# Optimization experiments

Measured on AMD Instinct MI355X. Metric: run time of the kernel, lower is better.

Reference implementation:

```python
import jax, jax.numpy as jnp
import numpy as np

N, E, G = 100000, 1600000, 128
IN, HID, HEADS, EDIM, OUT = 16, 32, 4, 8, 4
HC = HEADS * HID


def _p(k, shape):
    return jax.random.normal(k, shape, jnp.float32) * 0.1


def setup_inputs():
    key = jax.random.key(0)
    ks = list(jax.random.split(key, 24))
    nxt = iter(ks)
    d = dict(
        x=jax.random.normal(next(nxt), (N, IN), jnp.float32),
        edge_index=jax.random.randint(next(nxt), (2, E), 0, N),
        edge_attr=jax.random.normal(next(nxt), (E, EDIM), jnp.float32),
        batch=jnp.sort(jax.random.randint(next(nxt), (N,), 0, G)),
    )
    # conv1: in=IN -> heads*hid
    d['wl1'] = _p(next(nxt), (IN, HC));  d['bl1'] = jnp.zeros((HC,), jnp.float32)
    d['wr1'] = _p(next(nxt), (IN, HC));  d['br1'] = jnp.zeros((HC,), jnp.float32)
    d['we1'] = _p(next(nxt), (EDIM, HC)); d['att1'] = _p(next(nxt), (HEADS, HID)); d['bc1'] = jnp.zeros((HC,), jnp.float32)
    # conv2: in=HC -> heads*hid
    d['wl2'] = _p(next(nxt), (HC, HC));  d['bl2'] = jnp.zeros((HC,), jnp.float32)
    d['wr2'] = _p(next(nxt), (HC, HC));  d['br2'] = jnp.zeros((HC,), jnp.float32)
    d['we2'] = _p(next(nxt), (EDIM, HC)); d['att2'] = _p(next(nxt), (HEADS, HID)); d['bc2'] = jnp.zeros((HC,), jnp.float32)
    # conv3: in=HC -> 1*hid (heads=1)
    d['wl3'] = _p(next(nxt), (HC, HID)); d['bl3'] = jnp.zeros((HID,), jnp.float32)
    d['wr3'] = _p(next(nxt), (HC, HID)); d['br3'] = jnp.zeros((HID,), jnp.float32)
    d['we3'] = _p(next(nxt), (EDIM, HID)); d['att3'] = _p(next(nxt), (1, HID)); d['bc3'] = jnp.zeros((HID,), jnp.float32)
    d['w_fc1'] = _p(next(nxt), (HID, 2 * HID)); d['b_fc1'] = jnp.zeros((2 * HID,), jnp.float32)
    d['w_fc2'] = _p(next(nxt), (2 * HID, OUT)); d['b_fc2'] = jnp.zeros((OUT,), jnp.float32)
    return d


def _gatv2(x, src, dst, eattr, wl, bl, wr, br, we, att, bias, n):
    # PyG GATv2Conv: e_ij = a^T . leaky_relu(Wl x_j + Wr x_i + We e_ij)
    H, C = att.shape
    xl = (x @ wl + bl).reshape(-1, H, C)  # source transform [N,H,C]
    xr = (x @ wr + br).reshape(-1, H, C)  # target transform [N,H,C]
    ea = (eattr @ we).reshape(-1, H, C)   # edge transform   [E,H,C]
    e = jax.nn.leaky_relu(xl[src] + xr[dst] + ea, 0.2)  # [E,H,C]
    logit = jnp.einsum('ehc,hc->eh', e, att)            # [E,H]
    m = jax.ops.segment_max(logit, dst, num_segments=n)
    p = jnp.exp(logit - m[dst])
    s = jax.ops.segment_sum(p, dst, num_segments=n)
    alpha = p / (s[dst] + 1e-16)                        # segment softmax per dst
    out = jax.ops.segment_sum(xl[src] * alpha[:, :, None], dst, num_segments=n)
    return out.reshape(n, H * C) + bias


def reference(x, edge_index, edge_attr, batch,
              wl1, bl1, wr1, br1, we1, att1, bc1,
              wl2, bl2, wr2, br2, we2, att2, bc2,
              wl3, bl3, wr3, br3, we3, att3, bc3,
              w_fc1, b_fc1, w_fc2, b_fc2):
    n = x.shape[0]
    src, dst = edge_index[0], edge_index[1]
    # add_self_loops=True with fill_value='mean' (mean of incoming edge_attr per node)
    ones_e = jnp.ones((src.shape[0],), x.dtype)
    cnt = jax.ops.segment_sum(ones_e, dst, num_segments=n)
    loop_attr = jax.ops.segment_sum(edge_attr, dst, num_segments=n) / jnp.maximum(cnt, 1.0)[:, None]
    ar = jnp.arange(n)
    src_a = jnp.concatenate([src, ar])
    dst_a = jnp.concatenate([dst, ar])
    ea = jnp.concatenate([edge_attr, loop_attr], axis=0)

    h = jax.nn.elu(_gatv2(x, src_a, dst_a, ea, wl1, bl1, wr1, br1, we1, att1, bc1, n))
    h = jax.nn.elu(_gatv2(h, src_a, dst_a, ea, wl2, bl2, wr2, br2, we2, att2, bc2, n))
    h = jax.nn.elu(_gatv2(h, src_a, dst_a, ea, wl3, bl3, wr3, br3, we3, att3, bc3, n))

    # global mean pool over graphs
    gs = jax.ops.segment_sum(h, batch, num_segments=G)
    gc = jax.ops.segment_sum(jnp.ones((n,), h.dtype), batch, num_segments=G)
    g = gs / jnp.maximum(gc, 1.0)[:, None]

    g = jax.nn.elu(g @ w_fc1 + b_fc1)
    return g @ w_fc2 + b_fc2
```

## Files before the change

kernel.cpp:

```cpp
#include <hip/hip_runtime.h>
#include <cstdint>
#include <type_traits>

constexpr int GNUM = 128;

typedef _Float16 h2 __attribute__((ext_vector_type(2)));
typedef _Float16 h4 __attribute__((ext_vector_type(4)));
typedef _Float16 h8 __attribute__((ext_vector_type(8)));
typedef float f4 __attribute__((ext_vector_type(4)));


__global__ __launch_bounds__(256) void hist_kernel(const int* __restrict__ dst,
                                                   int* __restrict__ cnt, int E) {
  int i = blockIdx.x * 256 + threadIdx.x;
  if (i < E) atomicAdd(&cnt[dst[i]], 1);
}

__global__ __launch_bounds__(256) void scan_part_kernel(const int* __restrict__ cnt,
                                                        int* __restrict__ bpart, int n) {
  __shared__ int red[256];
  int base = blockIdx.x * 512;
  int t = threadIdx.x;
  int s = 0;
  int i0 = base + t, i1 = base + 256 + t;
  if (i0 < n) s += cnt[i0] + 1;
  if (i1 < n) s += cnt[i1] + 1;
  red[t] = s;
  __syncthreads();
  for (int off = 128; off > 0; off >>= 1) {
    if (t < off) red[t] += red[t + off];
    __syncthreads();
  }
  if (t == 0) bpart[blockIdx.x] = red[0];
}

__global__ __launch_bounds__(1024) void scan_top_kernel(const int* __restrict__ bpart,
                                                        int* __restrict__ boff,
                                                        int* __restrict__ row_ptr,
                                                        const int* __restrict__ batch,
                                                        int* __restrict__ gstart,
                                                        int B, int n) {
  __shared__ int buf[1024];
  int t = threadIdx.x;
  buf[t] = (t < B) ? bpart[t] : 0;
  __syncthreads();
  for (int off = 1; off < 1024; off <<= 1) {
    int v = (t >= off) ? buf[t - off] : 0;
    __syncthreads();
    buf[t] += v;
    __syncthreads();
  }
  if (t < B) boff[t] = (t == 0) ? 0 : buf[t - 1];
  if (t == 0) row_ptr[n] = buf[1023];
  if (t <= GNUM) {
    int lo = 0, hi = n;
    while (lo < hi) {
      int mid = (lo + hi) >> 1;
      if (batch[mid] < t) lo = mid + 1; else hi = mid;
    }
    gstart[t] = lo;
  }
}

__global__ __launch_bounds__(256) void scan_write_kernel(const int* __restrict__ cnt,
                                                         const int* __restrict__ boff,
                                                         int* __restrict__ row_ptr,
                                                         int* __restrict__ fill, int n) {
  __shared__ int red[256];
  int base = blockIdx.x * 512;
  int t = threadIdx.x;
  int i0 = base + 2 * t, i1 = base + 2 * t + 1;
  int v0 = (i0 < n) ? cnt[i0] + 1 : 0;
  int v1 = (i1 < n) ? cnt[i1] + 1 : 0;
  int val = v0 + v1;
  red[t] = val;
  __syncthreads();
  for (int off = 1; off < 256; off <<= 1) {
    int u = (t >= off) ? red[t - off] : 0;
    __syncthreads();
    red[t] += u;
    __syncthreads();
  }
  int o = boff[blockIdx.x] + red[t] - val;
  if (i0 < n) { row_ptr[i0] = o; fill[i0] = o; }
  if (i1 < n) { row_ptr[i1] = o + v0; fill[i1] = o + v0; }
}

__global__ __launch_bounds__(256) void scatter_kernel(const int* __restrict__ src,
                                                      const int* __restrict__ dst,
                                                      const float* __restrict__ ea,
                                                      int* __restrict__ fill,
                                                      int* __restrict__ csr_src,
                                                      _Float16* __restrict__ ea_csr, int E) {
  int i = blockIdx.x * 256 + threadIdx.x;
  if (i >= E) return;
  int d = dst[i];
  int p = atomicAdd(&fill[d], 1);
  csr_src[p] = src[i];
  float4 e0 = *(const float4*)&ea[(size_t)i * 8];
  float4 e1 = *(const float4*)&ea[(size_t)i * 8 + 4];
  h8 v;
  v[0] = (_Float16)e0.x; v[1] = (_Float16)e0.y; v[2] = (_Float16)e0.z; v[3] = (_Float16)e0.w;
  v[4] = (_Float16)e1.x; v[5] = (_Float16)e1.y; v[6] = (_Float16)e1.z; v[7] = (_Float16)e1.w;
  *(h8*)&ea_csr[(size_t)p * 8] = v;
}

__global__ __launch_bounds__(256) void selfloop_kernel(const int* __restrict__ row_ptr,
                                                       int* __restrict__ csr_src,
                                                       _Float16* __restrict__ ea_csr, int n) {
  int idx = blockIdx.x * 256 + threadIdx.x;
  int i = idx >> 3, c = idx & 7;
  if (i >= n) return;
  int s = row_ptr[i], e = row_ptr[i + 1] - 1;
  float a = 0.f;
  for (int j = s; j < e; j++) a += (float)ea_csr[(size_t)j * 8 + c];
  float inv = 1.f / fmaxf((float)(e - s), 1.f);
  ea_csr[(size_t)e * 8 + c] = (_Float16)(a * inv);
  if (c == 0) csr_src[e] = i;
}

__global__ __launch_bounds__(256) void pack_all_kernel(
    const float* __restrict__ wl1, _Float16* __restrict__ p1l,
    const float* __restrict__ wr1, _Float16* __restrict__ p1r,
    const float* __restrict__ wl2, _Float16* __restrict__ p2l,
    const float* __restrict__ wr2, _Float16* __restrict__ p2r,
    const float* __restrict__ wl3, _Float16* __restrict__ p3l,
    const float* __restrict__ wr3, _Float16* __restrict__ p3r) {
  int y = blockIdx.y;
  const float* w; _Float16* wp; int Kreal, Kpad, NC;
  switch (y) {
    case 0: w = wl1; wp = p1l; Kreal = 16;  Kpad = 32;  NC = 128; break;
    case 1: w = wr1; wp = p1r; Kreal = 16;  Kpad = 32;  NC = 128; break;
    case 2: w = wl2; wp = p2l; Kreal = 128; Kpad = 128; NC = 128; break;
    case 3: w = wr2; wp = p2r; Kreal = 128; Kpad = 128; NC = 128; break;
    case 4: w = wl3; wp = p3l; Kreal = 128; Kpad = 128; NC = 32;  break;
    default: w = wr3; wp = p3r; Kreal = 128; Kpad = 128; NC = 32; break;
  }
  int KB = Kpad / 32;
  int total = (NC / 16) * KB * 64;
  int idx = blockIdx.x * 256 + threadIdx.x;
  if (idx >= total) return;
  int lane = idx & 63;
  int blk = idx >> 6;
  int nt = blk / KB, kb = blk % KB;
  int col = nt * 16 + (lane & 15);
  int krow = kb * 32 + (lane >> 4) * 8;
  h8 v;
#pragma unroll
  for (int j = 0; j < 8; j++)
    v[j] = (krow + j < Kreal) ? (_Float16)w[(size_t)(krow + j) * NC + col] : (_Float16)0.f;
  *(h8*)&wp[(size_t)idx * 8] = v;
}


template <int K, int NCOLS>
__global__ __launch_bounds__(256) void k1m_kernel(const _Float16* __restrict__ x,
                                                  const _Float16* __restrict__ wp0,
                                                  const float* __restrict__ b0,
                                                  _Float16* __restrict__ out0,
                                                  const _Float16* __restrict__ wp1,
                                                  const float* __restrict__ b1,
                                                  _Float16* __restrict__ out1, int n) {
  constexpr int NT = NCOLS / 16, KB = K / 32;
  const _Float16* wp = blockIdx.y ? wp1 : wp0;
  const float* b = blockIdx.y ? b1 : b0;
  _Float16* out = blockIdx.y ? out1 : out0;

  int tid = threadIdx.x;
  int wave = tid >> 6, lane = tid & 63;
  int m = lane & 15, quad = lane >> 4;
  int node0 = blockIdx.x * 64 + wave * 16;

  h8 afrag[KB];
  int anode = node0 + m;
  if (anode < n) {
#pragma unroll
    for (int kb = 0; kb < KB; kb++)
      afrag[kb] = *(const h8*)&x[(size_t)anode * K + kb * 32 + quad * 8];
  } else {
#pragma unroll
    for (int kb = 0; kb < KB; kb++) afrag[kb] = (h8)(_Float16)0.f;
  }

  f4 acc[NT] = {};
#pragma unroll
  for (int nt = 0; nt < NT; nt++) {
#pragma unroll
    for (int kb = 0; kb < KB; kb++) {
      h8 bfrag = *(const h8*)&wp[((size_t)(nt * KB + kb) * 64 + lane) * 8];
      acc[nt] = __builtin_amdgcn_mfma_f32_16x16x32_f16(afrag[kb], bfrag, acc[nt], 0, 0, 0);
    }
  }

#pragma unroll
  for (int nt = 0; nt < NT; nt++) {
#pragma unroll
    for (int r = 0; r < 4; r++) {
      int row = node0 + quad * 4 + r;
      if (row < n) {
        int col = nt * 16 + m;
        out[(size_t)row * NCOLS + col] = (_Float16)(acc[nt][r] + b[col]);
      }
    }
  }
}

template <int NCOLS>
__global__ __launch_bounds__(256) void k1m16_kernel(const float* __restrict__ x,
                                                    const _Float16* __restrict__ wp0,
                                                    const float* __restrict__ b0,
                                                    _Float16* __restrict__ out0,
                                                    const _Float16* __restrict__ wp1,
                                                    const float* __restrict__ b1,
                                                    _Float16* __restrict__ out1, int n) {
  constexpr int NT = NCOLS / 16;
  const _Float16* wp = blockIdx.y ? wp1 : wp0;
  const float* b = blockIdx.y ? b1 : b0;
  _Float16* out = blockIdx.y ? out1 : out0;

  int tid = threadIdx.x;
  int wave = tid >> 6, lane = tid & 63;
  int m = lane & 15, quad = lane >> 4;
  int node0 = blockIdx.x * 64 + wave * 16;

  int anode = node0 + m;
  h8 afrag = (h8)(_Float16)0.f;
  if (anode < n && quad < 2) {
    float4 v0 = *(const float4*)&x[(size_t)anode * 16 + quad * 8];
    float4 v1 = *(const float4*)&x[(size_t)anode * 16 + quad * 8 + 4];
    afrag[0] = (_Float16)v0.x; afrag[1] = (_Float16)v0.y;
    afrag[2] = (_Float16)v0.z; afrag[3] = (_Float16)v0.w;
    afrag[4] = (_Float16)v1.x; afrag[5] = (_Float16)v1.y;
    afrag[6] = (_Float16)v1.z; afrag[7] = (_Float16)v1.w;
  }

  f4 acc[NT] = {};
#pragma unroll
  for (int nt = 0; nt < NT; nt++) {
    h8 bfrag = *(const h8*)&wp[((size_t)nt * 64 + lane) * 8];
    acc[nt] = __builtin_amdgcn_mfma_f32_16x16x32_f16(afrag, bfrag, acc[nt], 0, 0, 0);
  }

#pragma unroll
  for (int nt = 0; nt < NT; nt++) {
#pragma unroll
    for (int r = 0; r < 4; r++) {
      int row = node0 + quad * 4 + r;
      if (row < n) {
        int col = nt * 16 + m;
        out[(size_t)row * NCOLS + col] = (_Float16)(acc[nt][r] + b[col]);
      }
    }
  }
}

template <int H>
__global__ __launch_bounds__(128) void k2_kernel(
    const _Float16* __restrict__ xl, const _Float16* __restrict__ xr,
    const int* __restrict__ row_ptr, const int* __restrict__ csr_src,
    const _Float16* __restrict__ ea_csr, const float* __restrict__ we,
    const float* __restrict__ att, const float* __restrict__ bc,
    _Float16* __restrict__ out, int n) {
  constexpr int HC = H * 32;
  constexpr int NL = HC / 4;
  constexpr int NPB = 128 / NL;

  int tid = threadIdx.x;
  int ln = tid / NL, q = tid % NL;
  int c0 = 4 * q;
  int node = blockIdx.x * NPB + ln;
  if (node >= n) return;

  h2 w2[8][2];
#pragma unroll
  for (int k = 0; k < 8; k++) {
    float4 v = *(const float4*)&we[k * HC + c0];
    w2[k][0] = h2{(_Float16)v.x, (_Float16)v.y};
    w2[k][1] = h2{(_Float16)v.z, (_Float16)v.w};
  }
  const float LOG2E = 1.44269504088896f;
  float4 av = *(const float4*)&att[c0];
  h2 a0 = h2{(_Float16)(av.x * LOG2E), (_Float16)(av.y * LOG2E)};
  h2 a1 = h2{(_Float16)(av.z * LOG2E), (_Float16)(av.w * LOG2E)};
  h4 xrh = *(const h4*)&xr[(size_t)node * HC + c0];
  h2 xr0 = h2{xrh[0], xrh[1]}, xr1 = h2{xrh[2], xrh[3]};
  const h2 p2 = h2{(_Float16)0.2f, (_Float16)0.2f};

  float acc[4] = {0.f, 0.f, 0.f, 0.f};
  float s = 0.f;

  int start = row_ptr[node], end = row_ptr[node + 1];
  int len = end - start;
  int pairs = (len + 1) >> 1;

  int j1 = (start + 1 < end) ? start + 1 : start;
  float m1 = (start + 1 < end) ? 1.f : 0.f;
  int s0 = csr_src[start], s1 = csr_src[j1];
  h8 e0 = *(const h8*)&ea_csr[(size_t)start * 8];
  h8 e1 = *(const h8*)&ea_csr[(size_t)j1 * 8];
  h4 x0 = *(const h4*)&xl[(size_t)s0 * HC + c0];
  h4 x1 = *(const h4*)&xl[(size_t)s1 * HC + c0];

#pragma unroll 2
  for (int p = 0; p < pairs; p++) {
    int jn = start + 2 * (p + 1);
    int k0 = (jn < end) ? jn : start;
    int k1 = (jn + 1 < end) ? jn + 1 : k0;
    float nm1 = (jn + 1 < end) ? 1.f : 0.f;
    int ns0 = csr_src[k0], ns1 = csr_src[k1];
    h8 ne0 = *(const h8*)&ea_csr[(size_t)k0 * 8];
    h8 ne1 = *(const h8*)&ea_csr[(size_t)k1 * 8];

    h2 t00 = h2{x0[0], x0[1]} + xr0;
    h2 t01 = h2{x0[2], x0[3]} + xr1;
    h2 t10 = h2{x1[0], x1[1]} + xr0;
    h2 t11 = h2{x1[2], x1[3]} + xr1;
#pragma unroll
    for (int k = 0; k < 8; k++) {
      h2 ev0 = h2{e0[k], e0[k]};
      h2 ev1 = h2{e1[k], e1[k]};
      t00 += ev0 * w2[k][0];
      t01 += ev0 * w2[k][1];
      t10 += ev1 * w2[k][0];
      t11 += ev1 * w2[k][1];
    }
    t00 = __builtin_elementwise_max(t00, t00 * p2);
    t01 = __builtin_elementwise_max(t01, t01 * p2);
    t10 = __builtin_elementwise_max(t10, t10 * p2);
    t11 = __builtin_elementwise_max(t11, t11 * p2);
    h2 pd0 = t00 * a0 + t01 * a1;
    h2 pd1 = t10 * a0 + t11 * a1;
    float part0 = (float)pd0[0] + (float)pd0[1];
    float part1 = (float)pd1[0] + (float)pd1[1];

    h4 nx0 = *(const h4*)&xl[(size_t)ns0 * HC + c0];
    h4 nx1 = *(const h4*)&xl[(size_t)ns1 * HC + c0];

    part0 += __shfl_xor(part0, 1, 64);
    part1 += __shfl_xor(part1, 1, 64);
    part0 += __shfl_xor(part0, 2, 64);
    part1 += __shfl_xor(part1, 2, 64);
    part0 += __shfl_xor(part0, 4, 64);
    part1 += __shfl_xor(part1, 4, 64);
    float pe0 = __builtin_amdgcn_exp2f(part0);
    float pe1 = __builtin_amdgcn_exp2f(part1) * m1;
    s += pe0 + pe1;
#pragma unroll
    for (int i = 0; i < 4; i++)
      acc[i] += pe0 * (float)x0[i] + pe1 * (float)x1[i];

    s0 = ns0; s1 = ns1; e0 = ne0; e1 = ne1; x0 = nx0; x1 = nx1; m1 = nm1;
  }

  float inv = 1.f / (s + 1e-16f);
  h4 o;
#pragma unroll
  for (int i = 0; i < 4; i++) {
    float v = acc[i] * inv + bc[c0 + i];
    o[i] = (_Float16)(v > 0.f ? v : (__expf(v) - 1.f));
  }
  *(h4*)&out[(size_t)node * HC + c0] = o;
}

__global__ __launch_bounds__(256) void poolfc_kernel(const _Float16* __restrict__ h,
                                                     const int* __restrict__ gstart,
                                                     const float* __restrict__ w1,
                                                     const float* __restrict__ b1,
                                                     const float* __restrict__ w2,
                                                     const float* __restrict__ b2,
                                                     float* __restrict__ out) {
  __shared__ float red[256];
  __shared__ float g[32];
  __shared__ float a1[64];
  int gi = blockIdx.x;
  int t = threadIdx.x;
  int s = gstart[gi], e = gstart[gi + 1];
  int c = t & 31, rg = t >> 5;
  float acc = 0.f;
  for (int i = s + rg; i < e; i += 8) acc += (float)h[(size_t)i * 32 + c];
  red[t] = acc;
  __syncthreads();
  if (t < 128) red[t] += red[t + 128];
  __syncthreads();
  if (t < 64) red[t] += red[t + 64];
  __syncthreads();
  if (t < 32) g[t] = (red[t] + red[t + 32]) / fmaxf((float)(e - s), 1.f);
  __syncthreads();
  if (t < 64) {
    float v = b1[t];
    for (int k = 0; k < 32; k++) v += g[k] * w1[k * 64 + t];
    a1[t] = v > 0.f ? v : (__expf(v) - 1.f);
  }
  __syncthreads();
  if (t < 4) {
    float o = b2[t];
    for (int k = 0; k < 64; k++) o += a1[k] * w2[k * 4 + t];
    out[gi * 4 + t] = o;
  }
}


extern "C" void kernel_launch(void* const* d_in, const int* in_sizes, int n_in,
                              void* d_out, int out_size, void* d_ws, size_t ws_size,
                              hipStream_t stream) {
  const float* x     = (const float*)d_in[0];
  const int*   ei    = (const int*)d_in[1];
  const float* eattr = (const float*)d_in[2];
  const int*   batch = (const int*)d_in[3];
  const float *wl1 = (const float*)d_in[4],  *bl1 = (const float*)d_in[5];
  const float *wr1 = (const float*)d_in[6],  *br1 = (const float*)d_in[7];
  const float *we1 = (const float*)d_in[8],  *at1 = (const float*)d_in[9];
  const float *bc1 = (const float*)d_in[10];
  const float *wl2 = (const float*)d_in[11], *bl2 = (const float*)d_in[12];
  const float *wr2 = (const float*)d_in[13], *br2 = (const float*)d_in[14];
  const float *we2 = (const float*)d_in[15], *at2 = (const float*)d_in[16];
  const float *bc2 = (const float*)d_in[17];
  const float *wl3 = (const float*)d_in[18], *bl3 = (const float*)d_in[19];
  const float *wr3 = (const float*)d_in[20], *br3 = (const float*)d_in[21];
  const float *we3 = (const float*)d_in[22], *at3 = (const float*)d_in[23];
  const float *bc3 = (const float*)d_in[24];
  const float *wf1 = (const float*)d_in[25], *bf1 = (const float*)d_in[26];
  const float *wf2 = (const float*)d_in[27], *bf2 = (const float*)d_in[28];

  int N = in_sizes[0] / 16;
  int E = in_sizes[1] / 2;
  const int* srcp = ei;
  const int* dstp = ei + E;
  int EA = E + N;
  int NB = (N + 511) / 512;

  char* wsb = (char*)d_ws;
  size_t off = 0;
  auto alloc = [&](size_t bytes) -> char* {
    char* p = wsb + off;
    off += (bytes + 255) & ~(size_t)255;
    return p;
  };
  int*       cnt     = (int*)alloc((size_t)N * 4);
  int*       row_ptr = (int*)alloc((size_t)(N + 1) * 4);
  int*       fill    = (int*)alloc((size_t)N * 4);
  int*       bpart   = (int*)alloc((size_t)1024 * 4);
  int*       boff    = (int*)alloc((size_t)1024 * 4);
  int*       csr_src = (int*)alloc((size_t)EA * 4);
  _Float16*  ea_csr  = (_Float16*)alloc((size_t)EA * 8 * 2);
  _Float16*  xl      = (_Float16*)alloc((size_t)N * 128 * 2);
  _Float16*  xr      = (_Float16*)alloc((size_t)N * 128 * 2);
  _Float16*  h16     = (_Float16*)alloc((size_t)N * 128 * 2);
  _Float16*  h3      = (_Float16*)alloc((size_t)N * 32 * 2);
  int*       gstart  = (int*)alloc((size_t)(GNUM + 1) * 4);
  _Float16*  wp1l    = (_Float16*)alloc((size_t)32 * 128 * 2);
  _Float16*  wp1r    = (_Float16*)alloc((size_t)32 * 128 * 2);
  _Float16*  wp2l    = (_Float16*)alloc((size_t)128 * 128 * 2);
  _Float16*  wp2r    = (_Float16*)alloc((size_t)128 * 128 * 2);
  _Float16*  wp3l    = (_Float16*)alloc((size_t)128 * 32 * 2);
  _Float16*  wp3r    = (_Float16*)alloc((size_t)128 * 32 * 2);

  hipMemsetAsync(cnt, 0, (size_t)N * 4, stream);

  hist_kernel<<<(E + 255) / 256, 256, 0, stream>>>(dstp, cnt, E);
  scan_part_kernel<<<NB, 256, 0, stream>>>(cnt, bpart, N);
  scan_top_kernel<<<1, 1024, 0, stream>>>(bpart, boff, row_ptr, batch, gstart, NB, N);
  scan_write_kernel<<<NB, 256, 0, stream>>>(cnt, boff, row_ptr, fill, N);
  scatter_kernel<<<(E + 255) / 256, 256, 0, stream>>>(srcp, dstp, eattr, fill, csr_src, ea_csr, E);
  selfloop_kernel<<<(N * 8 + 255) / 256, 256, 0, stream>>>(row_ptr, csr_src, ea_csr, N);
  pack_all_kernel<<<dim3(8, 6), 256, 0, stream>>>(wl1, wp1l, wr1, wp1r,
                                                  wl2, wp2l, wr2, wp2r,
                                                  wl3, wp3l, wr3, wp3r);

  k1m16_kernel<128><<<dim3((N + 63) / 64, 2), 256, 0, stream>>>(
      x, wp1l, bl1, xl, wp1r, br1, xr, N);
  k2_kernel<4><<<(N + 3) / 4, 128, 0, stream>>>(xl, xr, row_ptr, csr_src, ea_csr,
                                                we1, at1, bc1, h16, N);
  k1m_kernel<128, 128><<<dim3((N + 63) / 64, 2), 256, 0, stream>>>(
      h16, wp2l, bl2, xl, wp2r, br2, xr, N);
  k2_kernel<4><<<(N + 3) / 4, 128, 0, stream>>>(xl, xr, row_ptr, csr_src, ea_csr,
                                                we2, at2, bc2, h16, N);
  k1m_kernel<128, 32><<<dim3((N + 63) / 64, 2), 256, 0, stream>>>(
      h16, wp3l, bl3, xl, wp3r, br3, xr, N);
  k2_kernel<1><<<(N + 15) / 16, 128, 0, stream>>>(xl, xr, row_ptr, csr_src, ea_csr,
                                                  we3, at3, bc3, h3, N);

  poolfc_kernel<<<GNUM, 256, 0, stream>>>(h3, gstart, wf1, bf1, wf2, bf2, (float*)d_out);
}
```

Before: 704.4 us.

## Use one-wavefront-per-node aggregation kernel for the four-head GATv2 layers

Adds a kernel that assigns a full 64-lane wavefront per destination node, with each lane handling two channels via packed half2 math. Source indices are read with readfirstlane, and the next pair of edges is prefetched while the current pair is computed, using an exp2-based softmax without max subtraction. It replaces the previous 32-lanes-per-node kernel for layers 1 and 2. This costs more threads per node and fp16 arithmetic for the logits, and skipping the max subtraction could overflow on large logits.

```diff
diff --git a/kernel.cpp b/kernel.cpp
--- a/kernel.cpp
+++ b/kernel.cpp
@@ -252,6 +252,120 @@
       }
     }
   }
+}
+
+__global__ __launch_bounds__(256) void k2w_kernel(
+    const _Float16* __restrict__ xl, const _Float16* __restrict__ xr,
+    const int* __restrict__ row_ptr, const int* __restrict__ csr_src,
+    const _Float16* __restrict__ ea_csr, const float* __restrict__ we,
+    const float* __restrict__ att, const float* __restrict__ bc,
+    _Float16* __restrict__ out, int n) {
+  int tid = threadIdx.x;
+  int lane = tid & 63;
+  int node = blockIdx.x * 4 + (tid >> 6);
+  if (node >= n) return;
+  int c0 = lane << 1;
+
+  h2 w2[8];
+#pragma unroll
+  for (int k = 0; k < 8; k++) {
+    float2 v = *(const float2*)&we[k * 128 + c0];
+    w2[k] = h2{(_Float16)v.x, (_Float16)v.y};
+  }
+  const float LOG2E = 1.44269504088896f;
+  float2 av = *(const float2*)&att[c0];
+  h2 a2 = h2{(_Float16)(av.x * LOG2E), (_Float16)(av.y * LOG2E)};
+  h2 xr2 = *(const h2*)&xr[(size_t)node * 128 + c0];
+  const h2 p2 = h2{(_Float16)0.2f, (_Float16)0.2f};
+
+  int start = __builtin_amdgcn_readfirstlane(row_ptr[node]);
+  int end   = __builtin_amdgcn_readfirstlane(row_ptr[node + 1]);
+
+  float s = 0.f, acc0 = 0.f, acc1 = 0.f;
+  int j = start;
+
+  if ((end - start) & 1) {
+    int s0 = __builtin_amdgcn_readfirstlane(csr_src[j]);
+    h8 e0 = *(const h8*)&ea_csr[(size_t)j * 8];
+    h2 x0 = *(const h2*)&xl[(uint32_t)s0 * 128u + (uint32_t)c0];
+    h2 t0 = x0 + xr2;
+#pragma unroll
+    for (int k = 0; k < 8; k++) t0 += h2{e0[k], e0[k]} * w2[k];
+    t0 = __builtin_elementwise_max(t0, t0 * p2);
+    h2 pd0 = t0 * a2;
+    float part0 = (float)pd0[0] + (float)pd0[1];
+    part0 += __shfl_xor(part0, 1, 64);
+    part0 += __shfl_xor(part0, 2, 64);
+    part0 += __shfl_xor(part0, 4, 64);
+    part0 += __shfl_xor(part0, 8, 64);
+    float pe0 = __builtin_amdgcn_exp2f(part0);
+    s += pe0;
+    acc0 += pe0 * (float)x0[0];
+    acc1 += pe0 * (float)x0[1];
+    j++;
+  }
+
+  if (j < end) {
+    int base = j;
+    int pairs = (end - j) >> 1;
+    int s0 = __builtin_amdgcn_readfirstlane(csr_src[j]);
+    int s1 = __builtin_amdgcn_readfirstlane(csr_src[j + 1]);
+    h8 e0 = *(const h8*)&ea_csr[(size_t)j * 8];
+    h8 e1 = *(const h8*)&ea_csr[((size_t)j + 1) * 8];
+    h2 x0 = *(const h2*)&xl[(uint32_t)s0 * 128u + (uint32_t)c0];
+    h2 x1 = *(const h2*)&xl[(uint32_t)s1 * 128u + (uint32_t)c0];
+
+#pragma unroll 2
+    for (int p = 0; p < pairs; p++) {
+      int jn = j + 2 * (p + 1);
+      int kp = (jn < end) ? jn : base;
+      int ns0 = __builtin_amdgcn_readfirstlane(csr_src[kp]);
+      int ns1 = __builtin_amdgcn_readfirstlane(csr_src[kp + 1]);
+      h8 ne0 = *(const h8*)&ea_csr[(size_t)kp * 8];
+      h8 ne1 = *(const h8*)&ea_csr[((size_t)kp + 1) * 8];
+
+      h2 t0 = x0 + xr2;
+      h2 t1 = x1 + xr2;
+#pragma unroll
+      for (int k = 0; k < 8; k++) {
+        t0 += h2{e0[k], e0[k]} * w2[k];
+        t1 += h2{e1[k], e1[k]} * w2[k];
+      }
+      t0 = __builtin_elementwise_max(t0, t0 * p2);
+      t1 = __builtin_elementwise_max(t1, t1 * p2);
+      h2 pd0 = t0 * a2;
+      h2 pd1 = t1 * a2;
+      float part0 = (float)pd0[0] + (float)pd0[1];
+      float part1 = (float)pd1[0] + (float)pd1[1];
+
+      h2 nx0 = *(const h2*)&xl[(uint32_t)ns0 * 128u + (uint32_t)c0];
+      h2 nx1 = *(const h2*)&xl[(uint32_t)ns1 * 128u + (uint32_t)c0];
+
+      part0 += __shfl_xor(part0, 1, 64);
+      part1 += __shfl_xor(part1, 1, 64);
+      part0 += __shfl_xor(part0, 2, 64);
+      part1 += __shfl_xor(part1, 2, 64);
+      part0 += __shfl_xor(part0, 4, 64);
+      part1 += __shfl_xor(part1, 4, 64);
+      part0 += __shfl_xor(part0, 8, 64);
+      part1 += __shfl_xor(part1, 8, 64);
+      float pe0 = __builtin_amdgcn_exp2f(part0);
+      float pe1 = __builtin_amdgcn_exp2f(part1);
+      s += pe0 + pe1;
+      acc0 += pe0 * (float)x0[0] + pe1 * (float)x1[0];
+      acc1 += pe0 * (float)x0[1] + pe1 * (float)x1[1];
+
+      e0 = ne0; e1 = ne1; x0 = nx0; x1 = nx1;
+    }
+  }
+
+  float inv = 1.f / (s + 1e-16f);
+  float2 bv = *(const float2*)&bc[c0];
+  float v0 = acc0 * inv + bv.x;
+  float v1 = acc1 * inv + bv.y;
+  v0 = v0 > 0.f ? v0 : (__expf(v0) - 1.f);
+  v1 = v1 > 0.f ? v1 : (__expf(v1) - 1.f);
+  *(h2*)&out[(size_t)node * 128 + c0] = h2{(_Float16)v0, (_Float16)v1};
 }
 
 template <int H>
@@ -469,12 +583,12 @@
 
   k1m16_kernel<128><<<dim3((N + 63) / 64, 2), 256, 0, stream>>>(
       x, wp1l, bl1, xl, wp1r, br1, xr, N);
-  k2_kernel<4><<<(N + 3) / 4, 128, 0, stream>>>(xl, xr, row_ptr, csr_src, ea_csr,
-                                                we1, at1, bc1, h16, N);
+  k2w_kernel<<<(N + 3) / 4, 256, 0, stream>>>(xl, xr, row_ptr, csr_src, ea_csr,
+                                              we1, at1, bc1, h16, N);
   k1m_kernel<128, 128><<<dim3((N + 63) / 64, 2), 256, 0, stream>>>(
       h16, wp2l, bl2, xl, wp2r, br2, xr, N);
-  k2_kernel<4><<<(N + 3) / 4, 128, 0, stream>>>(xl, xr, row_ptr, csr_src, ea_csr,
-                                                we2, at2, bc2, h16, N);
+  k2w_kernel<<<(N + 3) / 4, 256, 0, stream>>>(xl, xr, row_ptr, csr_src, ea_csr,
+                                              we2, at2, bc2, h16, N);
   k1m_kernel<128, 32><<<dim3((N + 63) / 64, 2), 256, 0, stream>>>(
       h16, wp3l, bl3, xl, wp3r, br3, xr, N);
   k2_kernel<1><<<(N + 15) / 16, 128, 0, stream>>>(xl, xr, row_ptr, csr_src, ea_csr,
```

Result: slower. 719.8 us (+2.2%).
